# Kernel tuning notes

Measured on AMD Instinct MI355X. Metric: run time of the kernel, lower is better.

## Reference

```python
import jax, jax.numpy as jnp
import numpy as np
import math

N = 100000          # total nodes across all subgraphs
E = 1600000         # directed edges (avg degree 16)
H = 128             # hidden_channels
MAXZ = 1000         # max_z
G = 1000            # number of subgraphs (unique batch ids)
NPG = N // G        # nodes per subgraph
L = 3               # num_layers


def setup_inputs() -> dict:
    key = jax.random.key(0)
    ks = jax.random.split(key, 9)
    z = jax.random.randint(ks[0], (N,), 0, MAXZ, dtype=jnp.int32)
    edge_index = jax.random.randint(ks[1], (2, E), 0, N, dtype=jnp.int32)
    batch = jnp.repeat(jnp.arange(G, dtype=jnp.int32), NPG)  # sorted graph ids
    s = 1.0 / math.sqrt(H)
    z_emb_table = jax.random.normal(ks[2], (MAXZ, H), jnp.float32) * 0.1
    conv_w = jax.random.normal(ks[3], (L, H, H), jnp.float32) * s
    conv_b = jnp.zeros((L, H), jnp.float32)
    mlp_w1 = jax.random.normal(ks[4], (H, H), jnp.float32) * s
    mlp_b1 = jnp.zeros((H,), jnp.float32)
    mlp_w2 = jax.random.normal(ks[5], (H, 1), jnp.float32) * s
    mlp_b2 = jnp.zeros((1,), jnp.float32)
    return {"num_nodes": N, "z": z, "edge_index": edge_index, "batch": batch,
            "z_emb_table": z_emb_table, "conv_w": conv_w, "conv_b": conv_b,
            "mlp_w1": mlp_w1, "mlp_b1": mlp_b1, "mlp_w2": mlp_w2, "mlp_b2": mlp_b2}


def reference(num_nodes, z, edge_index, batch, z_emb_table, conv_w, conv_b,
              mlp_w1, mlp_b1, mlp_w2, mlp_b2):
    # --- GCN normalization (PyG GCNConv: add self-loops, sym deg norm) ---
    loops = jnp.arange(num_nodes, dtype=edge_index.dtype)
    src = jnp.concatenate([edge_index[0], loops])  # [E+N]
    dst = jnp.concatenate([edge_index[1], loops])
    deg = jax.ops.segment_sum(jnp.ones_like(dst, jnp.float32), dst,
                              num_segments=num_nodes)
    dinv = jnp.where(deg > 0, jax.lax.rsqrt(deg), 0.0)
    norm = (dinv[src] * dinv[dst])[:, None]        # [E+N, 1]

    # --- embedding lookup (eval mode: no dropedge/dropout) ---
    x = z_emb_table[z]                             # [N, H]

    # --- stacked GCNConv: linear -> gather -> normalize -> scatter-add ---
    for l in range(L):
        h = x @ conv_w[l]                          # [N, H]
        h = jax.ops.segment_sum(h[src] * norm, dst, num_segments=num_nodes)
        h = h + conv_b[l]
        x = jax.nn.relu(h) if l < L - 1 else h

    # --- center-node pooling: first occurrence of each batch id ---
    first = jnp.concatenate([jnp.array([True]), batch[1:] != batch[:-1]])
    ci = jnp.nonzero(first, size=G)[0]             # [G]
    xs = x[ci] * x[ci + 1]                         # src * dst node features

    # --- MLP head [H, H, 1] (batch_norm=False, eval: dropout off) ---
    h = jax.nn.relu(xs @ mlp_w1 + mlp_b1)
    return h @ mlp_w2 + mlp_b2                     # [G, 1]
```

## Files before the change

kernel.cpp:

```cpp
#include <hip/hip_runtime.h>
#include <hip/hip_fp16.h>

#define HD 128
#define BSH 9
#define NBLKA 256
#define CAP 96
#define EDSCAP 10240
#define CAPB 12288
#define XSW(row, c8) (((size_t)(row) << 7) + ((size_t)(((c8) ^ ((row) & 7))) << 3))

typedef _Float16 half8_t __attribute__((ext_vector_type(8)));
typedef float floatx4 __attribute__((ext_vector_type(4)));

__device__ inline unsigned pack_h2(float x, float y) {
  __half2 h = __floats2half2_rn(x, y);
  return __builtin_bit_cast(unsigned, h);
}
__device__ inline float2 up_h2(unsigned u) {
  __half2 h = __builtin_bit_cast(__half2, u);
  return __half22float2(h);
}

__device__ inline void add8(float* acc, uint4 r) {
  float2 f;
  f = up_h2(r.x); acc[0] += f.x; acc[1] += f.y;
  f = up_h2(r.y); acc[2] += f.x; acc[3] += f.y;
  f = up_h2(r.z); acc[4] += f.x; acc[5] += f.y;
  f = up_h2(r.w); acc[6] += f.x; acc[7] += f.y;
}

__device__ inline void fma8w(float* acc, uint4 r, float w) {
  float2 f;
  f = up_h2(r.x); acc[0] = fmaf(w, f.x, acc[0]); acc[1] = fmaf(w, f.y, acc[1]);
  f = up_h2(r.y); acc[2] = fmaf(w, f.x, acc[2]); acc[3] = fmaf(w, f.y, acc[3]);
  f = up_h2(r.z); acc[4] = fmaf(w, f.x, acc[4]); acc[5] = fmaf(w, f.y, acc[5]);
  f = up_h2(r.w); acc[6] = fmaf(w, f.x, acc[6]); acc[7] = fmaf(w, f.y, acc[7]);
}

__global__ __launch_bounds__(256) void k_phase0(const int* __restrict__ src,
                                                const int* __restrict__ dst, int E, int nbuck,
                                                unsigned* __restrict__ bpool,
                                                int* __restrict__ counts,
                                                const float* __restrict__ conv_w,
                                                uint4* __restrict__ wfrag,
                                                const int* __restrict__ batch,
                                                int* __restrict__ ci,
                                                int* __restrict__ flag,
                                                int n) {
  __shared__ int cnt[512];
  int b = blockIdx.x;
  if (b < NBLKA) {
    for (int i = threadIdx.x; i < nbuck; i += 256) cnt[i] = 0;
    __syncthreads();
    int chunk = (E + NBLKA - 1) / NBLKA;
    int lo = b * chunk, hi = min(E, lo + chunk);
    for (int i = lo + threadIdx.x; i < hi; i += 256) {
      int s = src[i], d = dst[i];
      int bk = d >> BSH;
      int c = atomicAdd(&cnt[bk], 1);
      if (c < CAP)
        bpool[((size_t)bk * NBLKA + b) * CAP + c] =
            ((unsigned)(d & ((1 << BSH) - 1)) << 23) | (unsigned)s;
    }
    __syncthreads();
    for (int bk = threadIdx.x; bk < nbuck; bk += 256) counts[(size_t)bk * NBLKA + b] = cnt[bk];
  } else if (b < NBLKA + 24) {
    int t = (b - NBLKA) * 256 + threadIdx.x;
    int lane = t & 63;
    int s = (t >> 6) & 3;
    int c4 = (t >> 8) & 3;
    int chalf = (t >> 10) & 1;
    int layer = t >> 11;
    int col = chalf * 64 + c4 * 16 + (lane & 15);
    int k0 = s * 32 + (lane >> 4) * 8;
    const float* W = conv_w + (size_t)layer * HD * HD;
    unsigned u[4];
#pragma unroll
    for (int j = 0; j < 4; ++j)
      u[j] = pack_h2(W[(size_t)(k0 + 2 * j) * HD + col], W[(size_t)(k0 + 2 * j + 1) * HD + col]);
    uint4 o; o.x = u[0]; o.y = u[1]; o.z = u[2]; o.w = u[3];
    wfrag[t] = o;
  } else {
    int i = (b - NBLKA - 24) * 256 + threadIdx.x;
    if (i >= n) return;
    flag[i] = 0;
    if (i == 0) flag[n] = 0;
    if (i == 0 || batch[i] != batch[i - 1]) ci[batch[i]] = i;
  }
}

__device__ inline void gemm16(const _Float16* xs, const uint4* __restrict__ wfragL,
                              const float* __restrict__ dinv, uint2* __restrict__ Yh,
                              int row0, int nvalid, const int* __restrict__ rowmap,
                              int tid) {
  int lane = tid & 63, w = tid >> 6;
  int chalf = w >> 1, h = lane >> 4;
  half8_t wf[8];
#pragma unroll
  for (int cc = 0; cc < 2; ++cc)
#pragma unroll
    for (int s = 0; s < 4; ++s) {
      int c4 = 2 * (w & 1) + cc;
      wf[cc * 4 + s] = __builtin_bit_cast(half8_t,
          wfragL[((chalf * 4 + c4) * 4 + s) * 64 + lane]);
    }
  half8_t bf[4];
#pragma unroll
  for (int s = 0; s < 4; ++s)
    bf[s] = *(const half8_t*)&xs[XSW(lane & 15, s * 4 + h)];
  floatx4 acc[2];
  acc[0] = (floatx4){0.f, 0.f, 0.f, 0.f};
  acc[1] = (floatx4){0.f, 0.f, 0.f, 0.f};
#pragma unroll
  for (int s = 0; s < 4; ++s) {
    acc[0] = __builtin_amdgcn_mfma_f32_16x16x32_f16(wf[s], bf[s], acc[0], 0, 0, 0);
    acc[1] = __builtin_amdgcn_mfma_f32_16x16x32_f16(wf[4 + s], bf[s], acc[1], 0, 0, 0);
  }
  int i = row0 + (lane & 15);
  if (i < nvalid) {
    int orow = rowmap ? rowmap[i] : i;
    float dv = dinv ? dinv[orow] : 1.0f;
#pragma unroll
    for (int cc = 0; cc < 2; ++cc) {
      int c4 = 2 * (w & 1) + cc;
      int colbase = chalf * 64 + c4 * 16 + h * 4;
      uint2 o;
      o.x = pack_h2(acc[cc][0] * dv, acc[cc][1] * dv);
      o.y = pack_h2(acc[cc][2] * dv, acc[cc][3] * dv);
      Yh[(size_t)orow * 32 + (colbase >> 2)] = o;
    }
  }
}

__global__ __launch_bounds__(256) void k_build(const unsigned* __restrict__ bpool,
                                               const int* __restrict__ counts,
                                               int n, int nbuck, int maxz,
                                               const int* __restrict__ z,
                                               const float4* __restrict__ emb,
                                               const uint4* __restrict__ wfrag0,
                                               float* __restrict__ dinv,
                                               uint2* __restrict__ d2,
                                               uint2* __restrict__ t0,
                                               int* __restrict__ rowstart,
                                               int* __restrict__ rowend,
                                               int* __restrict__ col) {
  __shared__ __align__(16) unsigned eds[EDSCAP];
  __shared__ int hist[1 << BSH];
  __shared__ int wsum[256];
  __shared__ int coff[NBLKA + 1];
  int b = blockIdx.x;
  int t = threadIdx.x;
  if (b >= nbuck) {
    int rb = b - nbuck;
    _Float16* xs = (_Float16*)eds;
    int grp = t >> 4, li = t & 15;
    int row = rb * 16 + grp;
    int r = row < maxz ? row : maxz - 1;
    const float4* er = emb + (size_t)r * 32 + li * 2;
    float4 f0 = er[0], f1 = er[1];
    uint4 hx;
    hx.x = pack_h2(f0.x, f0.y); hx.y = pack_h2(f0.z, f0.w);
    hx.z = pack_h2(f1.x, f1.y); hx.w = pack_h2(f1.z, f1.w);
    *(uint4*)&xs[XSW(grp, li)] = hx;
    __syncthreads();
    gemm16(xs, wfrag0, nullptr, t0, rb * 16, maxz, nullptr, t);
    return;
  }
  int v = (t < NBLKA) ? min(counts[(size_t)b * NBLKA + t], CAP) : 0;
  wsum[t] = v;
  __syncthreads();
  for (int off = 1; off < NBLKA; off <<= 1) {
    int x = (t >= off) ? wsum[t - off] : 0;
    __syncthreads();
    wsum[t] += x;
    __syncthreads();
  }
  if (t < NBLKA) coff[t] = wsum[t] - v;
  if (t == NBLKA - 1) coff[NBLKA] = wsum[NBLKA - 1];
  __syncthreads();
  int total = min(coff[NBLKA], EDSCAP);
  int w = t >> 6, lane = t & 63;
  for (int blk = w; blk < NBLKA; blk += 4) {
    int off0 = coff[blk], len = coff[blk + 1] - off0;
    const unsigned* seg = bpool + ((size_t)b * NBLKA + blk) * CAP;
    for (int i = lane; i < len; i += 64)
      if (off0 + i < EDSCAP) eds[off0 + i] = seg[i];
  }
  for (int i = t; i < (1 << BSH); i += 256) hist[i] = 0;
  __syncthreads();
  for (int i = t; i < total; i += 256) atomicAdd(&hist[eds[i] >> 23], 1);
  __syncthreads();
  int base = b << BSH;
  int nn = min(1 << BSH, n - base);
  int a0 = hist[2 * t], a1 = hist[2 * t + 1];
  int s = a0 + a1;
  wsum[t] = s;
  __syncthreads();
  for (int off = 1; off < 256; off <<= 1) {
    int x = (t >= off) ? wsum[t - off] : 0;
    __syncthreads();
    wsum[t] += x;
    __syncthreads();
  }
  int excl = wsum[t] - s;
  int cbase = b * CAPB;
  if (2 * t < nn) {
    int i = base + 2 * t;
    float d = 1.0f / sqrtf((float)(a0 + 1));
    rowstart[i] = cbase + excl;
    rowend[i] = cbase + excl + a0;
    dinv[i] = d;
    d2[i] = make_uint2((unsigned)z[i] * 16, __float_as_uint(d));
  }
  if (2 * t + 1 < nn) {
    int i = base + 2 * t + 1;
    float d = 1.0f / sqrtf((float)(a1 + 1));
    rowstart[i] = cbase + excl + a0;
    rowend[i] = cbase + excl + s;
    dinv[i] = d;
    d2[i] = make_uint2((unsigned)z[i] * 16, __float_as_uint(d));
  }
  hist[2 * t] = cbase + excl;
  hist[2 * t + 1] = cbase + excl + a0;
  __syncthreads();
  for (int i = t; i < total; i += 256) {
    unsigned pk = eds[i];
    int dl = pk >> 23;
    int pos = atomicAdd(&hist[dl], 1);
    col[pos] = (int)(pk & 0x7FFFFF);
  }
}

__global__ __launch_bounds__(64) void k_active(const int* __restrict__ ci,
                                               const int* __restrict__ rowstart,
                                               const int* __restrict__ rowend,
                                               const int* __restrict__ col,
                                               int g2, int* __restrict__ flag,
                                               int* __restrict__ list, int n) {
  int lane = threadIdx.x;
  int vid = blockIdx.x * 64 + lane;
  bool haveRow = vid < g2;
  int* nactive = flag + n;
  int node = 0, e = 0, end = 0;
  if (haveRow) {
    node = ci[vid >> 1] + (vid & 1);
    e = rowstart[node];
    end = rowend[node];
  }
  bool neu = haveRow && (atomicExch(&flag[node], 1) == 0);
  unsigned long long m = __ballot(neu);
  int base = 0;
  if (lane == 0 && m) base = atomicAdd(nactive, __popcll(m));
  base = __shfl(base, 0);
  if (neu) list[base + __popcll(m & ((1ULL << lane) - 1))] = node;
  for (;;) {
    bool act = haveRow && (e < end);
    if (!__any(act)) break;
    int s = act ? col[e] : 0;
    bool nw = act && (atomicExch(&flag[s], 1) == 0);
    unsigned long long mm = __ballot(nw);
    int b2 = 0;
    if (lane == 0 && mm) b2 = atomicAdd(nactive, __popcll(mm));
    b2 = __shfl(b2, 0);
    if (nw) list[b2 + __popcll(mm & ((1ULL << lane) - 1))] = s;
    ++e;
  }
}

__global__ __launch_bounds__(256) void k_agg0_gemm(const uint4* __restrict__ T0,
                                                   const uint2* __restrict__ D2,
                                                   const int* __restrict__ rowstart,
                                                   const int* __restrict__ rowend,
                                                   const int* __restrict__ col,
                                                   const float* __restrict__ dinv,
                                                   const float* __restrict__ bias,
                                                   const uint4* __restrict__ wfragL,
                                                   uint2* __restrict__ Yh, int n) {
  __shared__ __align__(16) _Float16 xs[16 * HD];
  int tid = threadIdx.x;
  int grp = tid >> 4, li = tid & 15;
  int node = blockIdx.x * 16 + grp;
  int nd = node < n ? node : n - 1;
  float acc[8] = {0.f, 0.f, 0.f, 0.f, 0.f, 0.f, 0.f, 0.f};
  uint2 ds = D2[nd];
  fma8w(acc, T0[ds.x + li], __uint_as_float(ds.y));
  int e = rowstart[nd], end = rowend[nd];
  for (; e + 3 < end; e += 4) {
    int c0 = col[e], c1 = col[e + 1], c2 = col[e + 2], c3 = col[e + 3];
    uint2 p0 = D2[c0], p1 = D2[c1], p2 = D2[c2], p3 = D2[c3];
    uint4 r0 = T0[p0.x + li];
    uint4 r1 = T0[p1.x + li];
    uint4 r2 = T0[p2.x + li];
    uint4 r3 = T0[p3.x + li];
    fma8w(acc, r0, __uint_as_float(p0.y));
    fma8w(acc, r1, __uint_as_float(p1.y));
    fma8w(acc, r2, __uint_as_float(p2.y));
    fma8w(acc, r3, __uint_as_float(p3.y));
  }
  for (; e < end; ++e) {
    uint2 p = D2[col[e]];
    fma8w(acc, T0[p.x + li], __uint_as_float(p.y));
  }
  float dv = dinv[nd];
  float4 b0 = ((const float4*)bias)[2 * li];
  float4 b1 = ((const float4*)bias)[2 * li + 1];
  acc[0] = fmaxf(fmaf(dv, acc[0], b0.x), 0.f);
  acc[1] = fmaxf(fmaf(dv, acc[1], b0.y), 0.f);
  acc[2] = fmaxf(fmaf(dv, acc[2], b0.z), 0.f);
  acc[3] = fmaxf(fmaf(dv, acc[3], b0.w), 0.f);
  acc[4] = fmaxf(fmaf(dv, acc[4], b1.x), 0.f);
  acc[5] = fmaxf(fmaf(dv, acc[5], b1.y), 0.f);
  acc[6] = fmaxf(fmaf(dv, acc[6], b1.z), 0.f);
  acc[7] = fmaxf(fmaf(dv, acc[7], b1.w), 0.f);
  uint4 hx;
  hx.x = pack_h2(acc[0], acc[1]); hx.y = pack_h2(acc[2], acc[3]);
  hx.z = pack_h2(acc[4], acc[5]); hx.w = pack_h2(acc[6], acc[7]);
  *(uint4*)&xs[XSW(grp, li)] = hx;
  __syncthreads();
  gemm16(xs, wfragL, dinv, Yh, blockIdx.x * 16, n, nullptr, tid);
}

__global__ __launch_bounds__(256) void k_agg_gemmL(const uint4* __restrict__ H,
                                                   const int* __restrict__ rowstart,
                                                   const int* __restrict__ rowend,
                                                   const int* __restrict__ col,
                                                   const float* __restrict__ dinv,
                                                   const float* __restrict__ bias,
                                                   const uint4* __restrict__ wfragL,
                                                   uint2* __restrict__ Yh,
                                                   const int* __restrict__ list,
                                                   const int* __restrict__ nactive) {
  __shared__ __align__(16) _Float16 xs[16 * HD];
  int na = *nactive;
  int tid = threadIdx.x;
  int grp = tid >> 4, li = tid & 15;
  for (int tile = blockIdx.x; tile * 16 < na; tile += gridDim.x) {
    int i = tile * 16 + grp;
    int node = list[i < na ? i : na - 1];
    uint4 srow = H[(size_t)node * 16 + li];
    float acc[8] = {0.f, 0.f, 0.f, 0.f, 0.f, 0.f, 0.f, 0.f};
    add8(acc, srow);
    int e = rowstart[node], end = rowend[node];
    for (; e + 3 < end; e += 4) {
      int c0 = col[e], c1 = col[e + 1], c2 = col[e + 2], c3 = col[e + 3];
      uint4 r0 = H[(size_t)c0 * 16 + li];
      uint4 r1 = H[(size_t)c1 * 16 + li];
      uint4 r2 = H[(size_t)c2 * 16 + li];
      uint4 r3 = H[(size_t)c3 * 16 + li];
      add8(acc, r0);
      add8(acc, r1);
      add8(acc, r2);
      add8(acc, r3);
    }
    for (; e < end; ++e) {
      uint4 r = H[(size_t)col[e] * 16 + li];
      add8(acc, r);
    }
    float dv = dinv[node];
    float4 b0 = ((const float4*)bias)[2 * li];
    float4 b1 = ((const float4*)bias)[2 * li + 1];
    acc[0] = fmaxf(fmaf(dv, acc[0], b0.x), 0.f);
    acc[1] = fmaxf(fmaf(dv, acc[1], b0.y), 0.f);
    acc[2] = fmaxf(fmaf(dv, acc[2], b0.z), 0.f);
    acc[3] = fmaxf(fmaf(dv, acc[3], b0.w), 0.f);
    acc[4] = fmaxf(fmaf(dv, acc[4], b1.x), 0.f);
    acc[5] = fmaxf(fmaf(dv, acc[5], b1.y), 0.f);
    acc[6] = fmaxf(fmaf(dv, acc[6], b1.z), 0.f);
    acc[7] = fmaxf(fmaf(dv, acc[7], b1.w), 0.f);
    uint4 hx;
    hx.x = pack_h2(acc[0], acc[1]); hx.y = pack_h2(acc[2], acc[3]);
    hx.z = pack_h2(acc[4], acc[5]); hx.w = pack_h2(acc[6], acc[7]);
    *(uint4*)&xs[XSW(grp, li)] = hx;
    __syncthreads();
    gemm16(xs, wfragL, dinv, Yh, tile * 16, na, list, tid);
    __syncthreads();
  }
}

__global__ __launch_bounds__(128) void k_tail(const uint4* __restrict__ H,
                                              const int* __restrict__ rowstart,
                                              const int* __restrict__ rowend,
                                              const int* __restrict__ col,
                                              const float* __restrict__ dinv,
                                              const float* __restrict__ bias,
                                              const int* __restrict__ ci,
                                              const float* __restrict__ W1,
                                              const float* __restrict__ b1,
                                              const float* __restrict__ w2,
                                              const float* __restrict__ b2,
                                              float* __restrict__ out, int G) {
  __shared__ float part[8][HD];
  __shared__ float xs[HD];
  __shared__ float red[HD];
  int g = blockIdx.x;
  int t = threadIdx.x;
  int grp = t >> 4, li = t & 15;
  int nodeA = ci[g];
  int node = nodeA + (grp >> 2);
  int gi = grp & 3;
  float acc[8] = {0.f, 0.f, 0.f, 0.f, 0.f, 0.f, 0.f, 0.f};
  if (gi == 0) add8(acc, H[(size_t)node * 16 + li]);
  for (int e = rowstart[node] + gi; e < rowend[node]; e += 4) {
    uint4 r = H[(size_t)col[e] * 16 + li];
    add8(acc, r);
  }
#pragma unroll
  for (int j = 0; j < 8; ++j) part[grp][li * 8 + j] = acc[j];
  __syncthreads();
  float sumA = part[0][t] + part[1][t] + part[2][t] + part[3][t];
  float sumB = part[4][t] + part[5][t] + part[6][t] + part[7][t];
  float bb = bias[t];
  float va = fmaf(dinv[nodeA], sumA, bb);
  float vb = fmaf(dinv[nodeA + 1], sumB, bb);
  xs[t] = va * vb;
  __syncthreads();
  float hacc = b1[t];
#pragma unroll 8
  for (int k = 0; k < HD; ++k) hacc = fmaf(xs[k], W1[k * HD + t], hacc);
  hacc = fmaxf(hacc, 0.f);
  red[t] = hacc * w2[t];
  __syncthreads();
  for (int off = 64; off > 0; off >>= 1) {
    if (t < off) red[t] += red[t + off];
    __syncthreads();
  }
  if (t == 0) out[g] = red[0] + b2[0];
}

extern "C" void kernel_launch(void* const* d_in, const int* in_sizes, int n_in,
                              void* d_out, int out_size, void* d_ws, size_t ws_size,
                              hipStream_t stream) {
  (void)n_in; (void)ws_size;
  const int*   z      = (const int*)d_in[1];
  const int*   ei     = (const int*)d_in[2];
  const int*   batch  = (const int*)d_in[3];
  const float* emb    = (const float*)d_in[4];
  const float* conv_w = (const float*)d_in[5];
  const float* conv_b = (const float*)d_in[6];
  const float* w1     = (const float*)d_in[7];
  const float* b1     = (const float*)d_in[8];
  const float* w2     = (const float*)d_in[9];
  const float* b2     = (const float*)d_in[10];
  int n = in_sizes[1];
  int E = in_sizes[2] / 2;
  int G = out_size;
  int maxz = in_sizes[4] / HD;
  const int* esrc = ei;
  const int* edst = ei + E;
  int nbuck = (n + (1 << BSH) - 1) >> BSH;
  int t0Blocks = (maxz + 15) / 16;

  char* p = (char*)d_ws;
  auto alloc = [&](size_t bytes) { void* r = (void*)p; p += (bytes + 255) / 256 * 256; return r; };
  unsigned* bufA     = (unsigned*)alloc((size_t)n * HD * 2);
  unsigned* bufB     = (unsigned*)alloc((size_t)n * HD * 2);
  float*    dinv     = (float*)alloc((size_t)n * 4);
  uint2*    d2       = (uint2*)alloc((size_t)n * 8);
  uint2*    t0       = (uint2*)alloc((size_t)(t0Blocks * 16) * 32 * 8);
  int*      rowstart = (int*)alloc((size_t)n * 4);
  int*      rowend   = (int*)alloc((size_t)n * 4);
  int*      col      = (int*)alloc((size_t)nbuck * CAPB * 4);
  uint4*    wfrag    = (uint4*)alloc((size_t)3 * 2048 * 16);
  int*      ci       = (int*)alloc((size_t)G * 4);
  int*      flag     = (int*)alloc((size_t)(n + 64) * 4);
  int*      list     = (int*)alloc((size_t)n * 4);
  unsigned* bpool    = (unsigned*)alloc((size_t)nbuck * NBLKA * CAP * 4);
  int*      counts   = (int*)alloc((size_t)nbuck * NBLKA * 4);

  int ciBlocks = (n + 255) / 256;
  int g2 = 2 * G;
  int* nactive = flag + n;

  k_phase0<<<NBLKA + 24 + ciBlocks, 256, 0, stream>>>(
      esrc, edst, E, nbuck, bpool, counts, conv_w, wfrag, batch, ci, flag, n);
  k_build<<<nbuck + t0Blocks, 256, 0, stream>>>(bpool, counts, n, nbuck, maxz, z,
                                                (const float4*)emb, wfrag, dinv, d2, t0,
                                                rowstart, rowend, col);
  k_active<<<(g2 + 63) / 64, 64, 0, stream>>>(ci, rowstart, rowend, col, g2, flag, list, n);
  k_agg0_gemm<<<(n + 15) / 16, 256, 0, stream>>>((const uint4*)t0, d2, rowstart, rowend, col,
                                                 dinv, conv_b, wfrag + 2048, (uint2*)bufA, n);
  k_agg_gemmL<<<512, 256, 0, stream>>>((const uint4*)bufA, rowstart, rowend, col, dinv,
                                       conv_b + HD, wfrag + 4096, (uint2*)bufB, list, nactive);
  k_tail<<<G, 128, 0, stream>>>((const uint4*)bufB, rowstart, rowend, col, dinv,
                                conv_b + 2 * HD, ci, w1, b1, w2, b2, (float*)d_out, G);
}
```

Baseline: 200.1 us.

## Sort nodes by degree bucket to balance layer-0 aggregation tiles

Builds a 64-bin in-degree histogram in k_build, then uses a new k_order kernel to counting-sort node ids by degree. The layer-0 aggregate+GEMM kernel processes nodes in that order, so the 16 rows sharing a block have similar edge counts and less lane divergence and tail imbalance. The active-set discovery is merged into the same launch, which removes one kernel launch. The cost is an extra pass over all nodes, global atomics, and scattered output writes through the order indirection.

```diff
diff --git a/kernel.cpp b/kernel.cpp
--- a/kernel.cpp
+++ b/kernel.cpp
@@ -46,6 +46,8 @@
                                                 const int* __restrict__ batch,
                                                 int* __restrict__ ci,
                                                 int* __restrict__ flag,
+                                                int* __restrict__ dhist,
+                                                int* __restrict__ dcur,
                                                 int n) {
   __shared__ int cnt[512];
   int b = blockIdx.x;
@@ -85,6 +87,7 @@
     if (i >= n) return;
     flag[i] = 0;
     if (i == 0) flag[n] = 0;
+    if (i < 64) { dhist[i] = 0; dcur[i] = 0; }
     if (i == 0 || batch[i] != batch[i - 1]) ci[batch[i]] = i;
   }
 }
@@ -143,11 +146,13 @@
                                                uint2* __restrict__ t0,
                                                int* __restrict__ rowstart,
                                                int* __restrict__ rowend,
-                                               int* __restrict__ col) {
+                                               int* __restrict__ col,
+                                               int* __restrict__ dhist) {
   __shared__ __align__(16) unsigned eds[EDSCAP];
   __shared__ int hist[1 << BSH];
   __shared__ int wsum[256];
   __shared__ int coff[NBLKA + 1];
+  __shared__ int h64[64];
   int b = blockIdx.x;
   int t = threadIdx.x;
   if (b >= nbuck) {
@@ -168,6 +173,7 @@
   }
   int v = (t < NBLKA) ? min(counts[(size_t)b * NBLKA + t], CAP) : 0;
   wsum[t] = v;
+  if (t < 64) h64[t] = 0;
   __syncthreads();
   for (int off = 1; off < NBLKA; off <<= 1) {
     int x = (t >= off) ? wsum[t - off] : 0;
@@ -211,6 +217,7 @@
     rowend[i] = cbase + excl + a0;
     dinv[i] = d;
     d2[i] = make_uint2((unsigned)z[i] * 16, __float_as_uint(d));
+    atomicAdd(&h64[min(a0, 63)], 1);
   }
   if (2 * t + 1 < nn) {
     int i = base + 2 * t + 1;
@@ -219,10 +226,12 @@
     rowend[i] = cbase + excl + s;
     dinv[i] = d;
     d2[i] = make_uint2((unsigned)z[i] * 16, __float_as_uint(d));
+    atomicAdd(&h64[min(a1, 63)], 1);
   }
   hist[2 * t] = cbase + excl;
   hist[2 * t + 1] = cbase + excl + a0;
   __syncthreads();
+  if (t < 64 && h64[t]) atomicAdd(&dhist[t], h64[t]);
   for (int i = t; i < total; i += 256) {
     unsigned pk = eds[i];
     int dl = pk >> 23;
@@ -231,39 +240,66 @@
   }
 }
 
-__global__ __launch_bounds__(64) void k_active(const int* __restrict__ ci,
-                                               const int* __restrict__ rowstart,
+__global__ __launch_bounds__(256) void k_order(const int* __restrict__ rowstart,
                                                const int* __restrict__ rowend,
                                                const int* __restrict__ col,
+                                               const int* __restrict__ dhist,
+                                               int* __restrict__ dcur,
+                                               int* __restrict__ order,
+                                               const int* __restrict__ ci,
                                                int g2, int* __restrict__ flag,
-                                               int* __restrict__ list, int n) {
-  int lane = threadIdx.x;
-  int vid = blockIdx.x * 64 + lane;
-  bool haveRow = vid < g2;
-  int* nactive = flag + n;
-  int node = 0, e = 0, end = 0;
-  if (haveRow) {
-    node = ci[vid >> 1] + (vid & 1);
-    e = rowstart[node];
-    end = rowend[node];
-  }
-  bool neu = haveRow && (atomicExch(&flag[node], 1) == 0);
-  unsigned long long m = __ballot(neu);
-  int base = 0;
-  if (lane == 0 && m) base = atomicAdd(nactive, __popcll(m));
-  base = __shfl(base, 0);
-  if (neu) list[base + __popcll(m & ((1ULL << lane) - 1))] = node;
-  for (;;) {
-    bool act = haveRow && (e < end);
-    if (!__any(act)) break;
-    int s = act ? col[e] : 0;
-    bool nw = act && (atomicExch(&flag[s], 1) == 0);
-    unsigned long long mm = __ballot(nw);
-    int b2 = 0;
-    if (lane == 0 && mm) b2 = atomicAdd(nactive, __popcll(mm));
-    b2 = __shfl(b2, 0);
-    if (nw) list[b2 + __popcll(mm & ((1ULL << lane) - 1))] = s;
-    ++e;
+                                               int* __restrict__ list, int n, int nob) {
+  int b = blockIdx.x;
+  int t = threadIdx.x;
+  if (b < nob) {
+    __shared__ int bassh[64];
+    __shared__ int lcnt[64], lbase[64];
+    if (t == 0) {
+      int s = 0;
+      for (int j = 0; j < 64; ++j) { bassh[j] = s; s += dhist[j]; }
+    }
+    if (t < 64) lcnt[t] = 0;
+    __syncthreads();
+    int i = b * 256 + t;
+    int bin = 0, r = 0;
+    bool valid = i < n;
+    if (valid) {
+      bin = min(rowend[i] - rowstart[i], 63);
+      r = atomicAdd(&lcnt[bin], 1);
+    }
+    __syncthreads();
+    if (t < 64) lbase[t] = lcnt[t] ? atomicAdd(&dcur[t], lcnt[t]) : 0;
+    __syncthreads();
+    if (valid) order[bassh[bin] + lbase[bin] + r] = i;
+  } else {
+    int lane = t & 63;
+    int vid = (b - nob) * 256 + t;
+    bool haveRow = vid < g2;
+    int* nactive = flag + n;
+    int node = 0, e = 0, end = 0;
+    if (haveRow) {
+      node = ci[vid >> 1] + (vid & 1);
+      e = rowstart[node];
+      end = rowend[node];
+    }
+    bool neu = haveRow && (atomicExch(&flag[node], 1) == 0);
+    unsigned long long m = __ballot(neu);
+    int base = 0;
+    if (lane == 0 && m) base = atomicAdd(nactive, __popcll(m));
+    base = __shfl(base, 0);
+    if (neu) list[base + __popcll(m & ((1ULL << lane) - 1))] = node;
+    for (;;) {
+      bool act = haveRow && (e < end);
+      if (!__any(act)) break;
+      int s = act ? col[e] : 0;
+      bool nw = act && (atomicExch(&flag[s], 1) == 0);
+      unsigned long long mm = __ballot(nw);
+      int b2 = 0;
+      if (lane == 0 && mm) b2 = atomicAdd(nactive, __popcll(mm));
+      b2 = __shfl(b2, 0);
+      if (nw) list[b2 + __popcll(mm & ((1ULL << lane) - 1))] = s;
+      ++e;
+    }
   }
 }
 
@@ -275,12 +311,13 @@
                                                    const float* __restrict__ dinv,
                                                    const float* __restrict__ bias,
                                                    const uint4* __restrict__ wfragL,
+                                                   const int* __restrict__ order,
                                                    uint2* __restrict__ Yh, int n) {
   __shared__ __align__(16) _Float16 xs[16 * HD];
   int tid = threadIdx.x;
   int grp = tid >> 4, li = tid & 15;
-  int node = blockIdx.x * 16 + grp;
-  int nd = node < n ? node : n - 1;
+  int i16 = blockIdx.x * 16 + grp;
+  int nd = order[i16 < n ? i16 : n - 1];
   float acc[8] = {0.f, 0.f, 0.f, 0.f, 0.f, 0.f, 0.f, 0.f};
   uint2 ds = D2[nd];
   fma8w(acc, T0[ds.x + li], __uint_as_float(ds.y));
@@ -317,7 +354,7 @@
   hx.z = pack_h2(acc[4], acc[5]); hx.w = pack_h2(acc[6], acc[7]);
   *(uint4*)&xs[XSW(grp, li)] = hx;
   __syncthreads();
-  gemm16(xs, wfragL, dinv, Yh, blockIdx.x * 16, n, nullptr, tid);
+  gemm16(xs, wfragL, dinv, Yh, blockIdx.x * 16, n, order, tid);
 }
 
 __global__ __launch_bounds__(256) void k_agg_gemmL(const uint4* __restrict__ H,
@@ -464,21 +501,28 @@
   int*      ci       = (int*)alloc((size_t)G * 4);
   int*      flag     = (int*)alloc((size_t)(n + 64) * 4);
   int*      list     = (int*)alloc((size_t)n * 4);
+  int*      order    = (int*)alloc((size_t)n * 4);
+  int*      dhist    = (int*)alloc(64 * 4);
+  int*      dcur     = (int*)alloc(64 * 4);
   unsigned* bpool    = (unsigned*)alloc((size_t)nbuck * NBLKA * CAP * 4);
   int*      counts   = (int*)alloc((size_t)nbuck * NBLKA * 4);
 
   int ciBlocks = (n + 255) / 256;
   int g2 = 2 * G;
+  int nob = (n + 255) / 256;
+  int actBlocks = (g2 + 255) / 256;
   int* nactive = flag + n;
 
   k_phase0<<<NBLKA + 24 + ciBlocks, 256, 0, stream>>>(
-      esrc, edst, E, nbuck, bpool, counts, conv_w, wfrag, batch, ci, flag, n);
+      esrc, edst, E, nbuck, bpool, counts, conv_w, wfrag, batch, ci, flag, dhist, dcur, n);
   k_build<<<nbuck + t0Blocks, 256, 0, stream>>>(bpool, counts, n, nbuck, maxz, z,
                                                 (const float4*)emb, wfrag, dinv, d2, t0,
-                                                rowstart, rowend, col);
-  k_active<<<(g2 + 63) / 64, 64, 0, stream>>>(ci, rowstart, rowend, col, g2, flag, list, n);
+                                                rowstart, rowend, col, dhist);
+  k_order<<<nob + actBlocks, 256, 0, stream>>>(rowstart, rowend, col, dhist, dcur, order,
+                                               ci, g2, flag, list, n, nob);
   k_agg0_gemm<<<(n + 15) / 16, 256, 0, stream>>>((const uint4*)t0, d2, rowstart, rowend, col,
-                                                 dinv, conv_b, wfrag + 2048, (uint2*)bufA, n);
+                                                 dinv, conv_b, wfrag + 2048, order,
+                                                 (uint2*)bufA, n);
   k_agg_gemmL<<<512, 256, 0, stream>>>((const uint4*)bufA, rowstart, rowend, col, dinv,
                                        conv_b + HD, wfrag + 4096, (uint2*)bufB, list, nactive);
   k_tail<<<G, 128, 0, stream>>>((const uint4*)bufB, rowstart, rowend, col, dinv,
```

Measured after the change: 209.5 us. 1.05x slower.
